# Performance work log

Hardware: AMD Instinct MI355X
Metric: run time of the kernel (lower is better)

Reference implementation:

```python
import jax, jax.numpy as jnp
import numpy as np

NUM_GRAPHS = 256
EPS = 1e-5
SLOPE = 0.01

def _lrelu(x):
    return jnp.where(x >= 0, x, SLOPE * x)

def _gcn(x, W, b, src, dst, ew, n_nodes):
    # GCNConv(normalize=False): out[dst] = sum_e ew[e] * (x @ W)[src[e]] + b
    h = x @ W
    msg = h[src] * ew[:, None]
    agg = jax.ops.segment_sum(msg, dst, num_segments=n_nodes)
    return agg + b

def _bn(x, g, beta):
    # training-mode BatchNorm1d over node dim, biased variance
    m = jnp.mean(x, axis=0)
    v = jnp.mean((x - m) ** 2, axis=0)
    return (x - m) * jax.lax.rsqrt(v + EPS) * g + beta

def setup_inputs() -> dict:
    key = jax.random.key(0)
    ks = jax.random.split(key, 20)
    N, E, F0 = 20000, 320000, 1280
    dims = [(F0, 640), (640, 512), (512, 256), (256, 256)]
    inp = {
        'x': jax.random.normal(ks[0], (N, F0), dtype=jnp.float32),
        'edge_index': jax.random.randint(ks[1], (2, E), 0, N, dtype=jnp.int64),
        'edge_weigth': jax.random.uniform(ks[2], (E,), dtype=jnp.float32),
        'batch': jnp.sort(jax.random.randint(ks[3], (N,), 0, NUM_GRAPHS, dtype=jnp.int64)),
    }
    for i, (fi, fo) in enumerate(dims, start=1):
        inp[f'W{i}'] = jax.random.normal(ks[3 + i], (fi, fo), dtype=jnp.float32) * (1.0 / np.sqrt(fi))
        inp[f'b{i}'] = jnp.zeros((fo,), dtype=jnp.float32)
        inp[f'g{i}'] = jnp.ones((fo,), dtype=jnp.float32)
        inp[f'be{i}'] = jnp.zeros((fo,), dtype=jnp.float32)
    fdims = [(256, 128), (128, 64), (64, 2)]
    for i, (fi, fo) in enumerate(fdims, start=1):
        inp[f'Wf{i}'] = jax.random.normal(ks[10 + i], (fi, fo), dtype=jnp.float32) * np.sqrt(2.0 / (fi + fo))
        inp[f'bf{i}'] = jnp.zeros((fo,), dtype=jnp.float32)
    return inp

def reference(x, edge_index, edge_weigth, batch,
              W1, b1, g1, be1, W2, b2, g2, be2,
              W3, b3, g3, be3, W4, b4, g4, be4,
              Wf1, bf1, Wf2, bf2, Wf3, bf3):
    n = x.shape[0]
    src, dst = edge_index[0], edge_index[1]
    h = _lrelu(_bn(_gcn(x, W1, b1, src, dst, edge_weigth, n), g1, be1))
    h = _lrelu(_bn(_gcn(h, W2, b2, src, dst, edge_weigth, n), g2, be2))
    h = _lrelu(_bn(_gcn(h, W3, b3, src, dst, edge_weigth, n), g3, be3))
    h = _lrelu(_bn(_gcn(h, W4, b4, src, dst, edge_weigth, n), g4, be4))
    pooled = jax.ops.segment_sum(h, batch, num_segments=NUM_GRAPHS)  # [G, 256]
    out = _lrelu(pooled @ Wf1 + bf1)
    out = _lrelu(out @ Wf2 + bf2)
    out = _lrelu(out @ Wf3 + bf3)
    return out
```

## Files before the change

### kernel.cpp

```cpp
#include <hip/hip_runtime.h>

typedef short bf16x8 __attribute__((ext_vector_type(8)));
typedef float f32x4  __attribute__((ext_vector_type(4)));

__device__ __forceinline__ float bf2f(unsigned short h){
  union { unsigned int u; float f; } c; c.u = ((unsigned int)h) << 16; return c.f;
}
__device__ __forceinline__ unsigned short f2bf(float f){
  union { float f; unsigned int u; } c; c.f = f;
  unsigned int u = c.u;
  return (unsigned short)((u + 0x7fffu + ((u >> 16) & 1u)) >> 16);
}
__device__ __forceinline__ void gload_lds16(const void* g, void* l){
  __builtin_amdgcn_global_load_lds((const __attribute__((address_space(1))) unsigned int*)g,
                                   (__attribute__((address_space(3))) unsigned int*)l, 16, 0, 0);
}
__device__ __forceinline__ float lrelu(float x){ return x >= 0.f ? x : 0.01f * x; }
__device__ __forceinline__ void acc2(float& a0, float& a1, unsigned int u, float w){
  float lo = __uint_as_float(u << 16);
  float hi = __uint_as_float(u & 0xffff0000u);
  a0 = fmaf(lo, w, a0); a1 = fmaf(hi, w, a1);
}

__global__ void cvt_f32_bf16(const float* __restrict__ x, unsigned short* __restrict__ o, int n4){
  int i = blockIdx.x * 256 + threadIdx.x;
  if (i >= n4) return;
  float4 v = ((const float4*)x)[i];
  ushort4 r; r.x = f2bf(v.x); r.y = f2bf(v.y); r.z = f2bf(v.z); r.w = f2bf(v.w);
  ((ushort4*)o)[i] = r;
}

__global__ void wt_kernel(const float* __restrict__ Wm, unsigned short* __restrict__ Wt, int K, int Nf){
  __shared__ float tile[32][33];
  int n0 = blockIdx.x * 32, k0 = blockIdx.y * 32;
  int tx = threadIdx.x, ty = threadIdx.y;
  for (int i = ty; i < 32; i += 8)
    tile[i][tx] = Wm[(size_t)(k0 + i) * Nf + n0 + tx];
  __syncthreads();
  for (int i = ty; i < 32; i += 8)
    Wt[(size_t)(n0 + i) * K + k0 + tx] = f2bf(tile[tx][i]);
}

__global__ void hist_kernel(const int* __restrict__ dst, int* __restrict__ hist, int E){
  int e = blockIdx.x * 256 + threadIdx.x;
  if (e < E) atomicAdd(&hist[dst[e]], 1);
}

__global__ void scan_kernel(int* __restrict__ hist, int* __restrict__ cursor, int n, int total){
  __shared__ int partials[1024];
  const int CH = 20;
  int t = threadIdx.x;
  int base = t * CH;
  int local[CH];
  int s = 0;
  for (int i = 0; i < CH; i++){
    int idx = base + i;
    int v = (idx < n) ? hist[idx] : 0;
    local[i] = s; s += v;
  }
  partials[t] = s;
  __syncthreads();
  for (int off = 1; off < 1024; off <<= 1){
    int v = (t >= off) ? partials[t - off] : 0;
    __syncthreads();
    if (t >= off) partials[t] += v;
    __syncthreads();
  }
  int pre = (t == 0) ? 0 : partials[t - 1];
  for (int i = 0; i < CH; i++){
    int idx = base + i;
    if (idx < n){ int v = pre + local[i]; hist[idx] = v; cursor[idx] = v; }
  }
  if (t == 0){ hist[n] = total; }
}

__global__ void scatter_kernel(const int* __restrict__ src, const int* __restrict__ dst,
                               const float* __restrict__ ew, int* __restrict__ cursor,
                               int* __restrict__ so, float* __restrict__ eo, int E){
  int e = blockIdx.x * 256 + threadIdx.x;
  if (e >= E) return;
  int d = dst[e];
  int p = atomicAdd(&cursor[d], 1);
  so[p] = src[e]; eo[p] = ew[e];
}

__global__ __launch_bounds__(256) void gemm_bf16(const unsigned short* __restrict__ A,
                                                 const unsigned short* __restrict__ Bt,
                                                 unsigned short* __restrict__ C,
                                                 int Nf, int K, int Nt){
  __shared__ unsigned short lsA[128 * 64];
  __shared__ unsigned short lsB[128 * 64];
  const int nwg = gridDim.x;
  const int orig = blockIdx.x;
  const int q = nwg >> 3, r = nwg & 7;
  const int xcd = orig & 7, idx = orig >> 3;
  const int wgid = (xcd < r ? xcd * (q + 1) : r * (q + 1) + (xcd - r) * q) + idx;
  const int mt = wgid / Nt, nt = wgid % Nt;

  const int tid = threadIdx.x;
  const int wave = tid >> 6, lane = tid & 63;
  const int wr = wave >> 1, wc = wave & 1;
  const size_t tm = (size_t)mt * 128, tn = (size_t)nt * 128;

  f32x4 acc[4][4] = {};

  const int lrow = lane >> 3;
  const int lcol = (lane & 7) * 8;
  const unsigned short* Ab = A  + (tm + wave * 32 + lrow) * (size_t)K + lcol;
  const unsigned short* Bb = Bt + (tn + wave * 32 + lrow) * (size_t)K + lcol;
  unsigned short* lA0 = &lsA[(wave * 32) * 64];
  unsigned short* lB0 = &lsB[(wave * 32) * 64];

  for (int k0 = 0; k0 < K; k0 += 64){
    #pragma unroll
    for (int s = 0; s < 4; s++){
      gload_lds16(Ab + (size_t)s * 8 * K + k0, lA0 + s * 8 * 64);
      gload_lds16(Bb + (size_t)s * 8 * K + k0, lB0 + s * 8 * 64);
    }
    __syncthreads();
    #pragma unroll
    for (int kk = 0; kk < 2; kk++){
      bf16x8 af[4], bfr[4];
      #pragma unroll
      for (int m = 0; m < 4; m++)
        af[m] = *(const bf16x8*)&lsA[(wr * 64 + m * 16 + (lane & 15)) * 64 + kk * 32 + (lane >> 4) * 8];
      #pragma unroll
      for (int n = 0; n < 4; n++)
        bfr[n] = *(const bf16x8*)&lsB[(wc * 64 + n * 16 + (lane & 15)) * 64 + kk * 32 + (lane >> 4) * 8];
      #pragma unroll
      for (int m = 0; m < 4; m++)
        #pragma unroll
        for (int n = 0; n < 4; n++)
          acc[m][n] = __builtin_amdgcn_mfma_f32_16x16x32_bf16(af[m], bfr[n], acc[m][n], 0, 0, 0);
    }
    __syncthreads();
  }
  #pragma unroll
  for (int m = 0; m < 4; m++)
    #pragma unroll
    for (int n = 0; n < 4; n++)
      #pragma unroll
      for (int j = 0; j < 4; j++){
        size_t row = tm + wr * 64 + m * 16 + (lane >> 4) * 4 + j;
        size_t col = tn + wc * 64 + n * 16 + (lane & 15);
        C[row * Nf + col] = f2bf(acc[m][n][j]);
      }
}

template<int F>
__global__ __launch_bounds__(256)
void agg_row(const unsigned short* __restrict__ H,
             const int* __restrict__ rp,
             const int* __restrict__ srcs,
             const float* __restrict__ ews,
             float* __restrict__ AGG, int Nnodes){
  const int wv = threadIdx.x >> 6, ln = threadIdx.x & 63;
  int node = blockIdx.x * 4 + wv;
  if (node >= Nnodes) return;
  node = __builtin_amdgcn_readfirstlane(node);
  const int e0 = rp[node], e1 = rp[node + 1];
  const unsigned int* Hd = (const unsigned int*)H;
  constexpr int RD = F / 2;

  float a0=0.f,a1=0.f,a2=0.f,a3=0.f,a4=0.f,a5=0.f,a6=0.f,a7=0.f,a8=0.f,a9=0.f;

  #define AGG_BODY(E) {                                            \
    int s_ = srcs[E]; float w_ = ews[E];                           \
    const unsigned int* row_ = Hd + (size_t)s_ * RD;               \
    if constexpr (F == 256){                                       \
      uint2 v_ = *(const uint2*)(row_ + ln * 2);                   \
      acc2(a0,a1,v_.x,w_); acc2(a2,a3,v_.y,w_);                    \
    } else if constexpr (F == 512){                                \
      uint4 v_ = *(const uint4*)(row_ + ln * 4);                   \
      acc2(a0,a1,v_.x,w_); acc2(a2,a3,v_.y,w_);                    \
      acc2(a4,a5,v_.z,w_); acc2(a6,a7,v_.w,w_);                    \
    } else {                                                       \
      uint4 v_ = *(const uint4*)(row_ + ln * 4);                   \
      unsigned int v2_ = row_[256 + ln];                           \
      acc2(a0,a1,v_.x,w_); acc2(a2,a3,v_.y,w_);                    \
      acc2(a4,a5,v_.z,w_); acc2(a6,a7,v_.w,w_);                    \
      acc2(a8,a9,v2_,w_);                                          \
    }                                                              \
  }

  int e = e0;
  for (; e + 1 < e1; e += 2){ AGG_BODY(e); AGG_BODY(e + 1); }
  if (e < e1) AGG_BODY(e);
  #undef AGG_BODY

  float* orow = AGG + (size_t)node * F;
  if constexpr (F == 256){
    float4 o = {a0, a1, a2, a3};
    *(float4*)(orow + ln * 4) = o;
  } else if constexpr (F == 512){
    float4 oA = {a0, a1, a2, a3}, oB = {a4, a5, a6, a7};
    *(float4*)(orow + ln * 8) = oA;
    *(float4*)(orow + ln * 8 + 4) = oB;
  } else {
    float4 oA = {a0, a1, a2, a3}, oB = {a4, a5, a6, a7};
    *(float4*)(orow + ln * 8) = oA;
    *(float4*)(orow + ln * 8 + 4) = oB;
    float2 oC = {a8, a9};
    *(float2*)(orow + 512 + ln * 2) = oC;
  }
}

__global__ void stats_kernel_v(const float* __restrict__ AGG, float* __restrict__ sum,
                               float* __restrict__ sumsq, int F){
  int nf4 = F >> 2;
  int f4 = blockIdx.x * 256 + threadIdx.x;
  if (f4 >= nf4) return;
  const float4* p = (const float4*)(AGG + (size_t)blockIdx.y * 500 * F) + f4;
  float4 s = {0.f,0.f,0.f,0.f}, q = {0.f,0.f,0.f,0.f};
  for (int r = 0; r < 500; r++){
    float4 v = p[(size_t)r * nf4];
    s.x += v.x; s.y += v.y; s.z += v.z; s.w += v.w;
    q.x += v.x*v.x; q.y += v.y*v.y; q.z += v.z*v.z; q.w += v.w*v.w;
  }
  atomicAdd(&sum[f4*4+0], s.x); atomicAdd(&sum[f4*4+1], s.y);
  atomicAdd(&sum[f4*4+2], s.z); atomicAdd(&sum[f4*4+3], s.w);
  atomicAdd(&sumsq[f4*4+0], q.x); atomicAdd(&sumsq[f4*4+1], q.y);
  atomicAdd(&sumsq[f4*4+2], q.z); atomicAdd(&sumsq[f4*4+3], q.w);
}

__global__ void norm_kernel_v2(const float* __restrict__ AGG, const float* __restrict__ sum,
                               const float* __restrict__ sumsq, const float* __restrict__ gw,
                               const float* __restrict__ bw, unsigned short* __restrict__ OUT,
                               int nf4, int total4){
  int i = blockIdx.x * 256 + threadIdx.x;
  if (i >= total4) return;
  int f4 = i % nf4;
  const float inv = 1.0f / 20000.0f;
  float4 s = ((const float4*)sum)[f4];
  float4 q = ((const float4*)sumsq)[f4];
  float4 g = ((const float4*)gw)[f4];
  float4 b = ((const float4*)bw)[f4];
  float4 a = ((const float4*)AGG)[i];
  ushort4 o;
  { float m = s.x * inv, v = fmaxf(q.x * inv - m * m, 0.f);
    o.x = f2bf(lrelu((a.x - m) * rsqrtf(v + 1e-5f) * g.x + b.x)); }
  { float m = s.y * inv, v = fmaxf(q.y * inv - m * m, 0.f);
    o.y = f2bf(lrelu((a.y - m) * rsqrtf(v + 1e-5f) * g.y + b.y)); }
  { float m = s.z * inv, v = fmaxf(q.z * inv - m * m, 0.f);
    o.z = f2bf(lrelu((a.z - m) * rsqrtf(v + 1e-5f) * g.z + b.z)); }
  { float m = s.w * inv, v = fmaxf(q.w * inv - m * m, 0.f);
    o.w = f2bf(lrelu((a.w - m) * rsqrtf(v + 1e-5f) * g.w + b.w)); }
  ((ushort4*)OUT)[i] = o;
}

__global__ void bounds_kernel(const int* __restrict__ batch, int* __restrict__ gstart, int n){
  int g = threadIdx.x;
  if (g > 256) return;
  int lo = 0, hi = n;
  while (lo < hi){ int mid = (lo + hi) >> 1; if (batch[mid] < g) lo = mid + 1; else hi = mid; }
  gstart[g] = lo;
}

__global__ __launch_bounds__(256) void pool_kernel_v(const unsigned short* __restrict__ A1,
                                                     const int* __restrict__ gstart,
                                                     float* __restrict__ pooled){
  int gph = blockIdx.x;
  int t = threadIdx.x;
  int c = t & 31, g = t >> 5;
  int r0 = gstart[gph], r1 = gstart[gph + 1];
  float acc[8] = {0.f,0.f,0.f,0.f,0.f,0.f,0.f,0.f};
  for (int r = r0 + g; r < r1; r += 8){
    bf16x8 v = *(const bf16x8*)&A1[(size_t)r * 256 + c * 8];
    #pragma unroll
    for (int j = 0; j < 8; j++) acc[j] += bf2f((unsigned short)v[j]);
  }
  __shared__ float red[8][256];
  if (g > 0){
    #pragma unroll
    for (int j = 0; j < 8; j++) red[g][c * 8 + j] = acc[j];
  }
  __syncthreads();
  if (g == 0){
    #pragma unroll
    for (int gg = 1; gg < 8; gg++)
      #pragma unroll
      for (int j = 0; j < 8; j++) acc[j] += red[gg][c * 8 + j];
    #pragma unroll
    for (int j = 0; j < 8; j++) pooled[gph * 256 + c * 8 + j] = acc[j];
  }
}

__global__ void fc_kernel(const float* __restrict__ pooled,
                          const float* __restrict__ Wf1, const float* __restrict__ bf1,
                          const float* __restrict__ Wf2, const float* __restrict__ bf2,
                          const float* __restrict__ Wf3, const float* __restrict__ bf3,
                          float* __restrict__ out){
  int g = blockIdx.x, t = threadIdx.x;
  __shared__ float p0[256], p1[128], p2[64];
  p0[t] = pooled[g * 256 + t];
  p0[t + 128] = pooled[g * 256 + t + 128];
  __syncthreads();
  float a = bf1[t];
  for (int k = 0; k < 256; k++) a += p0[k] * Wf1[k * 128 + t];
  p1[t] = lrelu(a);
  __syncthreads();
  if (t < 64){
    float a2 = bf2[t];
    for (int k = 0; k < 128; k++) a2 += p1[k] * Wf2[k * 64 + t];
    p2[t] = lrelu(a2);
  }
  __syncthreads();
  if (t < 2){
    float a3 = bf3[t];
    for (int k = 0; k < 64; k++) a3 += p2[k] * Wf3[k * 2 + t];
    out[g * 2 + t] = lrelu(a3);
  }
}

extern "C" void kernel_launch(void* const* d_in, const int* in_sizes, int n_in,
                              void* d_out, int out_size, void* d_ws, size_t ws_size,
                              hipStream_t stream){
  const int N = 20000, E = 320000;
  const float* x     = (const float*)d_in[0];
  const int*   ei    = (const int*)d_in[1];
  const float* ew    = (const float*)d_in[2];
  const int*   batch = (const int*)d_in[3];
  const float* W[4]  = {(const float*)d_in[4], (const float*)d_in[8], (const float*)d_in[12], (const float*)d_in[16]};
  const float* gw[4] = {(const float*)d_in[6], (const float*)d_in[10], (const float*)d_in[14], (const float*)d_in[18]};
  const float* bw[4] = {(const float*)d_in[7], (const float*)d_in[11], (const float*)d_in[15], (const float*)d_in[19]};
  const float* Wf1 = (const float*)d_in[20]; const float* bf1 = (const float*)d_in[21];
  const float* Wf2 = (const float*)d_in[22]; const float* bf2 = (const float*)d_in[23];
  const float* Wf3 = (const float*)d_in[24]; const float* bf3 = (const float*)d_in[25];

  const int Kd[4] = {1280, 640, 512, 256};
  const int Nd[4] = {640, 512, 256, 256};

  char* w = (char*)d_ws;
  unsigned short* XB = (unsigned short*)w;
  float* AGG = (float*)w;                 w += 51445760;
  unsigned short* H  = (unsigned short*)w; w += 25722880;
  unsigned short* A1 = (unsigned short*)w; w += 25722880;
  unsigned short* WT = (unsigned short*)w; w += 1638400;
  int*   hist   = (int*)w;   w += 80128;
  int*   cursor = (int*)w;   w += 80128;
  int*   srcs   = (int*)w;   w += 1280000;
  float* ews    = (float*)w; w += 1280000;
  float* sum    = (float*)w; w += 2560;
  float* sumsq  = (float*)w; w += 2560;
  int*   gstart = (int*)w;   w += 1280;
  float* pooled = (float*)w; w += 262144;
  (void)ws_size; (void)n_in; (void)in_sizes; (void)out_size;

  cvt_f32_bf16<<<(N * 1280 / 4 + 255) / 256, 256, 0, stream>>>(x, XB, N * 1280 / 4);

  hipMemsetAsync(hist, 0, 80128, stream);
  hist_kernel<<<E / 256, 256, 0, stream>>>(ei + E, hist, E);
  scan_kernel<<<1, 1024, 0, stream>>>(hist, cursor, N, E);
  scatter_kernel<<<E / 256, 256, 0, stream>>>(ei, ei + E, ew, cursor, srcs, ews, E);

  bounds_kernel<<<1, 320, 0, stream>>>(batch, gstart, N);

  const unsigned short* in = XB;
  for (int l = 0; l < 4; l++){
    int K = Kd[l], Nf = Nd[l];
    int Nt = Nf / 128;
    wt_kernel<<<dim3(Nf / 32, K / 32), dim3(32, 8), 0, stream>>>(W[l], WT, K, Nf);
    gemm_bf16<<<157 * Nt, 256, 0, stream>>>(in, WT, H, Nf, K, Nt);
    if (Nf == 640)      agg_row<640><<<(N + 3) / 4, 256, 0, stream>>>(H, hist, srcs, ews, AGG, N);
    else if (Nf == 512) agg_row<512><<<(N + 3) / 4, 256, 0, stream>>>(H, hist, srcs, ews, AGG, N);
    else                agg_row<256><<<(N + 3) / 4, 256, 0, stream>>>(H, hist, srcs, ews, AGG, N);
    hipMemsetAsync(sum, 0, 5120, stream);
    stats_kernel_v<<<dim3((Nf / 4 + 255) / 256, 40), 256, 0, stream>>>(AGG, sum, sumsq, Nf);
    int total4 = N * (Nf >> 2);
    norm_kernel_v2<<<(total4 + 255) / 256, 256, 0, stream>>>(AGG, sum, sumsq, gw[l], bw[l], A1, Nf >> 2, total4);
    in = A1;
  }

  pool_kernel_v<<<256, 256, 0, stream>>>(A1, gstart, pooled);
  fc_kernel<<<256, 128, 0, stream>>>(pooled, Wf1, bf1, Wf2, bf2, Wf3, bf3, (float*)d_out);
}
```

Measured before the change: 780.9 us.

## Double-buffer GEMM LDS tiles with XOR-swizzled layout and K-step of 32

```diff
diff --git a/kernel.cpp b/kernel.cpp
--- a/kernel.cpp
+++ b/kernel.cpp
@@ -88,8 +88,8 @@
                                                  const unsigned short* __restrict__ Bt,
                                                  unsigned short* __restrict__ C,
                                                  int Nf, int K, int Nt){
-  __shared__ unsigned short lsA[128 * 64];
-  __shared__ unsigned short lsB[128 * 64];
+  __shared__ unsigned short lsA[2][128 * 32];
+  __shared__ unsigned short lsB[2][128 * 32];
   const int nwg = gridDim.x;
   const int orig = blockIdx.x;
   const int q = nwg >> 3, r = nwg & 7;
@@ -104,37 +104,47 @@
 
   f32x4 acc[4][4] = {};
 
-  const int lrow = lane >> 3;
-  const int lcol = (lane & 7) * 8;
-  const unsigned short* Ab = A  + (tm + wave * 32 + lrow) * (size_t)K + lcol;
-  const unsigned short* Bb = Bt + (tn + wave * 32 + lrow) * (size_t)K + lcol;
-  unsigned short* lA0 = &lsA[(wave * 32) * 64];
-  unsigned short* lB0 = &lsB[(wave * 32) * 64];
-
-  for (int k0 = 0; k0 < K; k0 += 64){
-    #pragma unroll
-    for (int s = 0; s < 4; s++){
-      gload_lds16(Ab + (size_t)s * 8 * K + k0, lA0 + s * 8 * 64);
-      gload_lds16(Bb + (size_t)s * 8 * K + k0, lB0 + s * 8 * 64);
-    }
-    __syncthreads();
-    #pragma unroll
-    for (int kk = 0; kk < 2; kk++){
-      bf16x8 af[4], bfr[4];
-      #pragma unroll
-      for (int m = 0; m < 4; m++)
-        af[m] = *(const bf16x8*)&lsA[(wr * 64 + m * 16 + (lane & 15)) * 64 + kk * 32 + (lane >> 4) * 8];
+  const int srow = tid >> 2;
+  const int co = (((tid & 3) ^ (srow & 3)) * 8);
+  const unsigned short* Ab0 = A  + (tm + srow) * (size_t)K + co;
+  const unsigned short* Ab1 = A  + (tm + 64 + srow) * (size_t)K + co;
+  const unsigned short* Bb0 = Bt + (tn + srow) * (size_t)K + co;
+  const unsigned short* Bb1 = Bt + (tn + 64 + srow) * (size_t)K + co;
+
+  #define STAGE(b, k) {                                        \
+    gload_lds16(Ab0 + (k), &lsA[b][tid * 8]);                  \
+    gload_lds16(Ab1 + (k), &lsA[b][(tid + 256) * 8]);          \
+    gload_lds16(Bb0 + (k), &lsB[b][tid * 8]);                  \
+    gload_lds16(Bb1 + (k), &lsB[b][(tid + 256) * 8]);          \
+  }
+
+  STAGE(0, 0);
+  __syncthreads();
+
+  const int rchunk = (((lane >> 4) ^ (lane & 3)) * 8);
+  const int arow = wr * 64 + (lane & 15);
+  const int brow = wc * 64 + (lane & 15);
+
+  int cur = 0;
+  for (int k0 = 0; k0 < K; k0 += 32){
+    if (k0 + 32 < K) STAGE(cur ^ 1, k0 + 32);
+    bf16x8 af[4], bfr[4];
+    #pragma unroll
+    for (int m = 0; m < 4; m++)
+      af[m] = *(const bf16x8*)&lsA[cur][(arow + m * 16) * 32 + rchunk];
+    #pragma unroll
+    for (int n = 0; n < 4; n++)
+      bfr[n] = *(const bf16x8*)&lsB[cur][(brow + n * 16) * 32 + rchunk];
+    #pragma unroll
+    for (int m = 0; m < 4; m++)
       #pragma unroll
       for (int n = 0; n < 4; n++)
-        bfr[n] = *(const bf16x8*)&lsB[(wc * 64 + n * 16 + (lane & 15)) * 64 + kk * 32 + (lane >> 4) * 8];
-      #pragma unroll
-      for (int m = 0; m < 4; m++)
-        #pragma unroll
-        for (int n = 0; n < 4; n++)
-          acc[m][n] = __builtin_amdgcn_mfma_f32_16x16x32_bf16(af[m], bfr[n], acc[m][n], 0, 0, 0);
-    }
+        acc[m][n] = __builtin_amdgcn_mfma_f32_16x16x32_bf16(af[m], bfr[n], acc[m][n], 0, 0, 0);
     __syncthreads();
-  }
+    cur ^= 1;
+  }
+  #undef STAGE
+
   #pragma unroll
   for (int m = 0; m < 4; m++)
     #pragma unroll
```

Result: no change. 769.2 us (-1.5%).
